# Kernel optimization log

Measured on AMD Instinct MI355X. Metric: run time of the kernel, lower is better.

## Reference

```python
import jax, jax.numpy as jnp
import numpy as np

LAN_DIM = 2048
FEA_DIM = 128
N = 65536
SHRINK_THRES = 0.0025
R = 1.0
EPS = 1e-12


def setup_inputs() -> dict:
    key = jax.random.key(0)
    k1, k2 = jax.random.split(key)
    x = jax.random.normal(k1, (N, FEA_DIM), dtype=jnp.float32)
    # reset_parameters: uniform(-stdv, stdv), stdv = 1/sqrt(fea_dim)
    stdv = 1.0 / np.sqrt(FEA_DIM)
    weight = jax.random.uniform(k2, (LAN_DIM, FEA_DIM), dtype=jnp.float32,
                                minval=-stdv, maxval=stdv)
    return {"input": x, "weight": weight}


def reference(input, weight):
    x = input                                    # [N, D]
    logits = jnp.einsum('nd,ld->nl', x, weight)  # [N, L]
    att = jax.nn.softmax(logits, axis=1)
    # hard_shrink_relu
    shifted = att - SHRINK_THRES
    att = jax.nn.relu(shifted) * att / (jnp.abs(shifted) + EPS)
    # F.normalize(p=1, dim=1): x / max(||x||_1, eps); att is nonneg
    att = att / jnp.maximum(jnp.sum(att, axis=1, keepdims=True), EPS)
    output = jnp.einsum('nl,ld->nd', att, weight)  # [N, D]

    # nearest landmark: argmax over att per sample
    ind = jnp.argmax(att, axis=1)                # [N]
    nl = weight[ind]                             # [N, D]
    # second-nearest: overwrite each row's argmax entry with the row min, re-argmax
    row_min = jnp.min(att, axis=1)               # [N]
    att2 = att.at[jnp.arange(N), ind].set(row_min)
    ind2 = jnp.argmax(att2, axis=1)
    nl2 = weight[ind2]                           # [N, D]

    # center of codebook, samples within radius R (boolean mask instead of
    # data-dependent-length index list, for jit compatibility)
    cen = jnp.mean(weight, axis=0)               # [D]
    dist = jnp.sqrt(jnp.sum((x - cen[None, :]) ** 2, axis=1))
    col = dist < R                               # [N] bool

    return output, att, nl, nl2, col
```

## Files before the change

kernel.cpp:

```cpp
#include <hip/hip_runtime.h>
#include <math.h>

#define NS 65536
#define LAN 2048
#define FEA 128

constexpr float THRES = 0.0025f;
constexpr float FEPS  = 1e-12f;
constexpr int BM   = 32;
constexpr int MAXS = 63;

typedef _Float16 half8 __attribute__((ext_vector_type(8)));
typedef float    f32x4 __attribute__((ext_vector_type(4)));

__global__ void k_prep(const float* __restrict__ W,
                       _Float16* __restrict__ Wh, _Float16* __restrict__ Wl,
                       float* __restrict__ cen) {
    if (blockIdx.x < 1024) {
        int i = blockIdx.x * 256 + threadIdx.x;
        float w = W[i];
        _Float16 h = (_Float16)w;
        Wh[i] = h;
        Wl[i] = (_Float16)(w - (float)h);
    } else {
        __shared__ float sb[4];
        int k = blockIdx.x - 1024;
        int tid = threadIdx.x;
        float s = 0.f;
        for (int c = tid; c < LAN; c += 256) s += W[(size_t)c * FEA + k];
        #pragma unroll
        for (int off = 32; off >= 1; off >>= 1) s += __shfl_xor(s, off);
        if ((tid & 63) == 0) sb[tid >> 6] = s;
        __syncthreads();
        if (tid == 0) cen[k] = (sb[0] + sb[1] + sb[2] + sb[3]) * (1.0f / (float)LAN);
    }
}

__device__ static inline void gload_lds16(const void* g, void* l) {
    __builtin_amdgcn_global_load_lds(
        (const __attribute__((address_space(1))) void*)g,
        (__attribute__((address_space(3))) void*)l, 16, 0, 0);
}

__global__ __launch_bounds__(512, 2) void k_main(
    const float* __restrict__ X,
    const _Float16* __restrict__ Wh, const _Float16* __restrict__ Wl,
    const float* __restrict__ cen,
    float* __restrict__ o_att, float* __restrict__ o_col)
{
    __shared__ __align__(16) char s_pool[147456];
    __shared__ float s_red[8][BM];
    __shared__ float s_rsinv[BM], s_Sinv[BM];
    __shared__ int   s_cnt[BM];

    const int tid  = threadIdx.x;
    const int wv   = tid >> 6;
    const int lane = tid & 63;
    const int g    = lane >> 4;
    const int m    = lane & 15;
    const int row0 = blockIdx.x * BM;
    constexpr int XOFF = 131072;

    #define ISSUE_B(t_, buf_)                                                        \
        {                                                                            \
            const char* gh_ = (const char*)(Wh + (size_t)(wv * 256 + (t_) * 16) * FEA); \
            const char* gl_ = (const char*)(Wl + (size_t)(wv * 256 + (t_) * 16) * FEA); \
            char* lb_ = s_pool + (buf_) * 65536 + wv * 8192;                         \
            _Pragma("unroll")                                                        \
            for (int i_ = 0; i_ < 4; ++i_) {                                         \
                int c_ = i_ * 64 + lane;                                             \
                int gc_ = c_ ^ ((c_ >> 4) & 7);                                      \
                gload_lds16(gh_ + gc_ * 16, lb_ + i_ * 1024);                        \
            }                                                                        \
            _Pragma("unroll")                                                        \
            for (int i_ = 0; i_ < 4; ++i_) {                                         \
                int c_ = i_ * 64 + lane;                                             \
                int gc_ = c_ ^ ((c_ >> 4) & 7);                                      \
                gload_lds16(gl_ + gc_ * 16, lb_ + 4096 + i_ * 1024);                 \
            }                                                                        \
        }

    {
        const char* xg = (const char*)(X + (size_t)row0 * FEA);
        gload_lds16(xg + (wv * 2 + 0) * 1024 + lane * 16, s_pool + XOFF + (wv * 2 + 0) * 1024);
        gload_lds16(xg + (wv * 2 + 1) * 1024 + lane * 16, s_pool + XOFF + (wv * 2 + 1) * 1024);
    }
    ISSUE_B(0, 0)
    ISSUE_B(1, 1)
    asm volatile("s_waitcnt vmcnt(16)" ::: "memory");
    __builtin_amdgcn_s_barrier();
    __builtin_amdgcn_sched_barrier(0);

    half8 afh[2][4], afl[2][4];
    #pragma unroll
    for (int rt = 0; rt < 2; ++rt)
        #pragma unroll
        for (int kb = 0; kb < 4; ++kb) {
            const char* base = s_pool + XOFF + (rt * 16 + m) * 512 + (kb * 8 + g * 2) * 16;
            f32x4 xa = *(const f32x4*)(base);
            f32x4 xb = *(const f32x4*)(base + 16);
            half8 h, l;
            #pragma unroll
            for (int e = 0; e < 4; ++e) {
                _Float16 hh = (_Float16)xa[e];
                h[e] = hh; l[e] = (_Float16)(xa[e] - (float)hh);
            }
            #pragma unroll
            for (int e = 0; e < 4; ++e) {
                _Float16 hh = (_Float16)xb[e];
                h[4 + e] = hh; l[4 + e] = (_Float16)(xb[e] - (float)hh);
            }
            afh[rt][kb] = h; afl[rt][kb] = l;
        }

    #pragma unroll
    for (int u = 0; u < 4; ++u) {
        const int lr = wv * 4 + u;
        float2 x2 = *(const float2*)(s_pool + XOFF + lr * 512 + lane * 8);
        float dx0 = x2.x - cen[lane * 2];
        float dx1 = x2.y - cen[lane * 2 + 1];
        float dd = dx0 * dx0 + dx1 * dx1;
        #pragma unroll
        for (int off = 32; off >= 1; off >>= 1) dd += __shfl_xor(dd, off);
        if (lane == 0) o_col[row0 + lr] = (sqrtf(dd) < 1.0f) ? 1.0f : 0.0f;
    }

    f32x4 acc[2][16];
    #pragma unroll
    for (int rt = 0; rt < 2; ++rt)
        #pragma unroll
        for (int t = 0; t < 16; ++t) acc[rt][t] = (f32x4){0.f, 0.f, 0.f, 0.f};
    float ssum[2][4];
    #pragma unroll
    for (int rt = 0; rt < 2; ++rt)
        #pragma unroll
        for (int r = 0; r < 4; ++r) ssum[rt][r] = 0.f;

    #pragma unroll 16
    for (int t = 0; t < 16; ++t) {
        const int buf = t & 1;
        const char* bb = s_pool + buf * 65536 + wv * 8192;
        if (t < 15) { asm volatile("s_waitcnt vmcnt(12)" ::: "memory"); }
        else        { asm volatile("s_waitcnt vmcnt(4)"  ::: "memory"); }
        __builtin_amdgcn_sched_barrier(0);
        half8 bh[4];
        #pragma unroll
        for (int kb = 0; kb < 4; ++kb) {
            int off = (m * 256 + kb * 64 + g * 16) ^ ((m & 7) << 4);
            bh[kb] = *(const half8*)(bb + off);
        }
        asm volatile("s_waitcnt lgkmcnt(0)" ::: "memory");
        __builtin_amdgcn_sched_barrier(0);
        __builtin_amdgcn_s_setprio(1);
        #pragma unroll
        for (int kb = 0; kb < 4; ++kb)
            #pragma unroll
            for (int rt = 0; rt < 2; ++rt) {
                acc[rt][t] = __builtin_amdgcn_mfma_f32_16x16x32_f16(afh[rt][kb], bh[kb], acc[rt][t], 0, 0, 0);
                acc[rt][t] = __builtin_amdgcn_mfma_f32_16x16x32_f16(afl[rt][kb], bh[kb], acc[rt][t], 0, 0, 0);
            }
        __builtin_amdgcn_s_setprio(0);
        if (t < 15) { asm volatile("s_waitcnt vmcnt(8)" ::: "memory"); }
        else        { asm volatile("s_waitcnt vmcnt(0)" ::: "memory"); }
        __builtin_amdgcn_sched_barrier(0);
        half8 bl[4];
        #pragma unroll
        for (int kb = 0; kb < 4; ++kb) {
            int off = (m * 256 + kb * 64 + g * 16) ^ ((m & 7) << 4);
            bl[kb] = *(const half8*)(bb + 4096 + off);
        }
        asm volatile("s_waitcnt lgkmcnt(0)" ::: "memory");
        __builtin_amdgcn_sched_barrier(0);
        if (t < 14) ISSUE_B(t + 2, buf)
        __builtin_amdgcn_s_setprio(1);
        #pragma unroll
        for (int kb = 0; kb < 4; ++kb)
            #pragma unroll
            for (int rt = 0; rt < 2; ++rt)
                acc[rt][t] = __builtin_amdgcn_mfma_f32_16x16x32_f16(afh[rt][kb], bl[kb], acc[rt][t], 0, 0, 0);
        __builtin_amdgcn_s_setprio(0);
        #pragma unroll
        for (int rt = 0; rt < 2; ++rt)
            #pragma unroll
            for (int r = 0; r < 4; ++r) {
                float e = __expf(acc[rt][t][r]);
                acc[rt][t][r] = e;
                ssum[rt][r] += e;
            }
    }
    #undef ISSUE_B


    #pragma unroll
    for (int rt = 0; rt < 2; ++rt)
        #pragma unroll
        for (int r = 0; r < 4; ++r) {
            float s = ssum[rt][r];
            #pragma unroll
            for (int off = 8; off >= 1; off >>= 1) s += __shfl_xor(s, off);
            if (m == 0) s_red[wv][rt*16 + g*4 + r] = s;
        }
    __syncthreads();
    if (tid < BM) {
        float s = s_red[0][tid];
        #pragma unroll
        for (int w = 1; w < 8; ++w) s += s_red[w][tid];
        s_rsinv[tid] = 1.0f / s;
        s_cnt[tid] = 0;
    }
    __syncthreads();

    int*   s_scol = (int*)s_pool;
    float* s_sval = (float*)(s_pool + 16384);
    #pragma unroll
    for (int rt = 0; rt < 2; ++rt)
        #pragma unroll
        for (int r = 0; r < 4; ++r) {
            const int lr = rt*16 + g*4 + r;
            const float ri = s_rsinv[lr];
            float S = 0.f;
            #pragma unroll
            for (int t = 0; t < 16; ++t) {
                float soft = acc[rt][t][r] * ri;
                float sh = soft - THRES;
                if (sh > 0.f) {
                    float v = sh * soft / (sh + FEPS);
                    S += v;
                    int p = atomicAdd(&s_cnt[lr], 1);
                    if (p < MAXS) { s_scol[lr*64 + p] = wv*256 + t*16 + m; s_sval[lr*64 + p] = v; }
                }
            }
            #pragma unroll
            for (int off = 8; off >= 1; off >>= 1) S += __shfl_xor(S, off);
            if (m == 0) s_red[wv][lr] = S;
        }
    __syncthreads();
    if (tid < BM) {
        float S = s_red[0][tid];
        #pragma unroll
        for (int w = 1; w < 8; ++w) S += s_red[w][tid];
        s_Sinv[tid] = 1.0f / fmaxf(S, FEPS);
    }
    __syncthreads();

    {
        const int lrp = tid >> 4, j = tid & 15;
        const int cn = min(s_cnt[lrp], MAXS);
        const float si = s_Sinv[lrp];
        f32x4 vq, cq;
        #pragma unroll
        for (int e = 0; e < 4; ++e) {
            int p = j * 4 + e;
            if (p == 63) {
                vq[e] = 0.f;
                cq[e] = __int_as_float(cn);
            } else {
                bool live = p < cn;
                vq[e] = live ? s_sval[lrp*64 + p] * si : 0.f;
                cq[e] = __int_as_float(live ? s_scol[lrp*64 + p] : 0);
            }
        }
        float* base = o_att + (size_t)(row0 + lrp) * LAN;
        *(f32x4*)(base + j * 4)      = vq;
        *(f32x4*)(base + 64 + j * 4) = cq;
    }
}

__global__ __launch_bounds__(256) void k_att(
    const float* __restrict__ W,
    float* __restrict__ o_att, float* __restrict__ o_out,
    float* __restrict__ o_nl, float* __restrict__ o_nl2)
{
    __shared__ float s_att[8 * 2048];
    __shared__ float s_pack[8][128];
    __shared__ int   s_i1[8], s_i2[8];

    const int tid = threadIdx.x;
    const size_t rows0 = (size_t)blockIdx.x * 8;
    const int row = tid >> 5, q = tid & 31;

    *(f32x4*)&s_pack[row][q * 4] = *(const f32x4*)(o_att + (rows0 + row) * LAN + q * 4);
    __syncthreads();

    if (tid < 8) {
        const float* pk = s_pack[tid];
        const int cnt = __float_as_int(pk[64 + 63]);
        float t1v = -1.f, t2v = -1.f; int t1c = 0x7fffffff, t2c = 0x7fffffff;
        for (int p = 0; p < cnt; ++p) {
            float v = pk[p]; int c = __float_as_int(pk[64 + p]);
            if (v > t1v || (v == t1v && c < t1c)) {
                t2v = t1v; t2c = t1c; t1v = v; t1c = c;
            } else if (v > t2v || (v == t2v && c < t2c)) {
                t2v = v; t2c = c;
            }
        }
        s_i1[tid] = (cnt >= 1) ? t1c : 0;
        s_i2[tid] = (cnt >= 2) ? t2c : 0;
    }
    f32x4* sa4 = (f32x4*)s_att;
    #pragma unroll
    for (int e = 0; e < 16; ++e) sa4[e * 256 + tid] = (f32x4){0.f, 0.f, 0.f, 0.f};
    __syncthreads();

    {
        const int cnt = __float_as_int(s_pack[row][64 + 63]);
        #pragma unroll
        for (int h = 0; h < 2; ++h) {
            int p = q + h * 32;
            if (p < cnt) {
                float v = s_pack[row][p];
                int c = __float_as_int(s_pack[row][64 + p]);
                s_att[row * 2048 + c] = v;
            }
        }
        f32x4 o = (f32x4){0.f, 0.f, 0.f, 0.f};
        for (int p = 0; p < cnt; ++p) {
            float v = s_pack[row][p];
            int c = __float_as_int(s_pack[row][64 + p]);
            const f32x4 w4 = *(const f32x4*)(W + (size_t)c * FEA + q * 4);
            o += v * w4;
        }
        *(f32x4*)(o_out + (rows0 + row) * FEA + q * 4) = o;
        const int i1 = s_i1[row], i2 = s_i2[row];
        *(f32x4*)(o_nl  + (rows0 + row) * FEA + q * 4) = *(const f32x4*)(W + (size_t)i1 * FEA + q * 4);
        *(f32x4*)(o_nl2 + (rows0 + row) * FEA + q * 4) = *(const f32x4*)(W + (size_t)i2 * FEA + q * 4);
    }
    __syncthreads();

    float* gdst = o_att + rows0 * LAN;
    #pragma unroll
    for (int e = 0; e < 16; ++e) {
        int fi = e * 256 + tid;
        *(f32x4*)(gdst + (size_t)fi * 4) = sa4[fi];
    }
}

extern "C" void kernel_launch(void* const* d_in, const int* in_sizes, int n_in,
                              void* d_out, int out_size, void* d_ws, size_t ws_size,
                              hipStream_t stream) {
    const float* X = (const float*)d_in[0];
    const float* W = (const float*)d_in[1];

    _Float16* Wh = (_Float16*)d_ws;
    _Float16* Wl = Wh + (size_t)LAN * FEA;
    float*    cen = (float*)(Wl + (size_t)LAN * FEA);

    float* out      = (float*)d_out;
    float* o_output = out;
    float* o_att    = o_output + (size_t)NS * FEA;
    float* o_nl     = o_att    + (size_t)NS * LAN;
    float* o_nl2    = o_nl     + (size_t)NS * FEA;
    float* o_col    = o_nl2    + (size_t)NS * FEA;

    k_prep<<<1152, 256, 0, stream>>>(W, Wh, Wl, cen);
    k_main<<<NS / BM, 512, 0, stream>>>(X, Wh, Wl, cen, o_att, o_col);
    k_att<<<NS / 8, 256, 0, stream>>>(W, o_att, o_output, o_nl, o_nl2);
}
```

Baseline: 311.4 us.

## Process two row tiles per block, shrink LDS, read Wl from global

Each k_main block now handles 64 rows in two passes of 32, so the grid is half as large. The low-half weight Wl is read straight from global memory into registers rather than staged in LDS. The input low parts are kept in LDS instead of registers, which cuts the shared-memory footprint from about 147KB to about 106KB and frees registers. The B-high prefetch for the second pass is issued early, and the final att store in k_att uses nontemporal stores. In exchange, the global Wl loads are uncached by LDS and repeated across waves, and the extra barriers per pass add synchronisation.

```diff
diff --git a/kernel.cpp b/kernel.cpp
--- a/kernel.cpp
+++ b/kernel.cpp
@@ -7,7 +7,6 @@
 
 constexpr float THRES = 0.0025f;
 constexpr float FEPS  = 1e-12f;
-constexpr int BM   = 32;
 constexpr int MAXS = 63;
 
 typedef _Float16 half8 __attribute__((ext_vector_type(8)));
@@ -42,228 +41,255 @@
         (__attribute__((address_space(3))) void*)l, 16, 0, 0);
 }
 
+#define RAWBAR() { asm volatile("s_waitcnt lgkmcnt(0)" ::: "memory"); \
+                   __builtin_amdgcn_s_barrier(); \
+                   __builtin_amdgcn_sched_barrier(0); }
+
 __global__ __launch_bounds__(512, 2) void k_main(
     const float* __restrict__ X,
     const _Float16* __restrict__ Wh, const _Float16* __restrict__ Wl,
     const float* __restrict__ cen,
     float* __restrict__ o_att, float* __restrict__ o_col)
 {
-    __shared__ __align__(16) char s_pool[147456];
-    __shared__ float s_red[8][BM];
-    __shared__ float s_rsinv[BM], s_Sinv[BM];
-    __shared__ int   s_cnt[BM];
+    __shared__ __align__(16) char s_pool[106496];
+    __shared__ float s_red[8][32];
+    __shared__ float s_rsinv[32], s_Sinv[32];
+    __shared__ int   s_cnt[32];
 
     const int tid  = threadIdx.x;
     const int wv   = tid >> 6;
     const int lane = tid & 63;
     const int g    = lane >> 4;
     const int m    = lane & 15;
-    const int row0 = blockIdx.x * BM;
-    constexpr int XOFF = 131072;
-
-    #define ISSUE_B(t_, buf_)                                                        \
-        {                                                                            \
+    constexpr int XR0 = 65536, XR1 = 81920, AFL = 98304;
+
+    #define ISSUE_BH(t_, buf_)                                                      \
+        {                                                                           \
             const char* gh_ = (const char*)(Wh + (size_t)(wv * 256 + (t_) * 16) * FEA); \
-            const char* gl_ = (const char*)(Wl + (size_t)(wv * 256 + (t_) * 16) * FEA); \
-            char* lb_ = s_pool + (buf_) * 65536 + wv * 8192;                         \
-            _Pragma("unroll")                                                        \
-            for (int i_ = 0; i_ < 4; ++i_) {                                         \
-                int c_ = i_ * 64 + lane;                                             \
-                int gc_ = c_ ^ ((c_ >> 4) & 7);                                      \
-                gload_lds16(gh_ + gc_ * 16, lb_ + i_ * 1024);                        \
-            }                                                                        \
-            _Pragma("unroll")                                                        \
-            for (int i_ = 0; i_ < 4; ++i_) {                                         \
-                int c_ = i_ * 64 + lane;                                             \
-                int gc_ = c_ ^ ((c_ >> 4) & 7);                                      \
-                gload_lds16(gl_ + gc_ * 16, lb_ + 4096 + i_ * 1024);                 \
-            }                                                                        \
+            char* lb_ = s_pool + (buf_) * 32768 + wv * 4096;                        \
+            _Pragma("unroll")                                                       \
+            for (int i_ = 0; i_ < 4; ++i_) {                                        \
+                int c_ = i_ * 64 + lane;                                            \
+                int gc_ = c_ ^ ((c_ >> 4) & 7);                                     \
+                gload_lds16(gh_ + gc_ * 16, lb_ + i_ * 1024);                       \
+            }                                                                       \
         }
 
     {
-        const char* xg = (const char*)(X + (size_t)row0 * FEA);
-        gload_lds16(xg + (wv * 2 + 0) * 1024 + lane * 16, s_pool + XOFF + (wv * 2 + 0) * 1024);
-        gload_lds16(xg + (wv * 2 + 1) * 1024 + lane * 16, s_pool + XOFF + (wv * 2 + 1) * 1024);
-    }
-    ISSUE_B(0, 0)
-    ISSUE_B(1, 1)
-    asm volatile("s_waitcnt vmcnt(16)" ::: "memory");
+        const char* xg = (const char*)(X + (size_t)blockIdx.x * 64 * FEA);
+        gload_lds16(xg + (wv * 2 + 0) * 1024 + lane * 16, s_pool + XR0 + (wv * 2 + 0) * 1024);
+        gload_lds16(xg + (wv * 2 + 1) * 1024 + lane * 16, s_pool + XR0 + (wv * 2 + 1) * 1024);
+        gload_lds16(xg + 16384 + (wv * 2 + 0) * 1024 + lane * 16, s_pool + XR1 + (wv * 2 + 0) * 1024);
+        gload_lds16(xg + 16384 + (wv * 2 + 1) * 1024 + lane * 16, s_pool + XR1 + (wv * 2 + 1) * 1024);
+    }
+    asm volatile("s_waitcnt vmcnt(2)" ::: "memory");
     __builtin_amdgcn_s_barrier();
     __builtin_amdgcn_sched_barrier(0);
 
-    half8 afh[2][4], afl[2][4];
-    #pragma unroll
-    for (int rt = 0; rt < 2; ++rt)
-        #pragma unroll
-        for (int kb = 0; kb < 4; ++kb) {
-            const char* base = s_pool + XOFF + (rt * 16 + m) * 512 + (kb * 8 + g * 2) * 16;
-            f32x4 xa = *(const f32x4*)(base);
-            f32x4 xb = *(const f32x4*)(base + 16);
-            half8 h, l;
+    for (int pass = 0; pass < 2; ++pass) {
+        const int row0 = blockIdx.x * 64 + pass * 32;
+        const int XR = pass ? XR1 : XR0;
+
+        half8 afh[2][4];
+        #pragma unroll
+        for (int rt = 0; rt < 2; ++rt)
+            #pragma unroll
+            for (int kb = 0; kb < 4; ++kb) {
+                const char* base = s_pool + XR + (rt * 16 + m) * 512 + (kb * 32 + g * 8) * 4;
+                f32x4 xa = *(const f32x4*)(base);
+                f32x4 xb = *(const f32x4*)(base + 16);
+                half8 h, l;
+                #pragma unroll
+                for (int e = 0; e < 4; ++e) {
+                    _Float16 hh = (_Float16)xa[e];
+                    h[e] = hh; l[e] = (_Float16)(xa[e] - (float)hh);
+                }
+                #pragma unroll
+                for (int e = 0; e < 4; ++e) {
+                    _Float16 hh = (_Float16)xb[e];
+                    h[4 + e] = hh; l[4 + e] = (_Float16)(xb[e] - (float)hh);
+                }
+                afh[rt][kb] = h;
+                int ab = (((rt * 16 + m) * 256 + kb * 64 + g * 16) ^ ((m & 7) << 4));
+                *(half8*)(s_pool + AFL + ab) = l;
+            }
+
+        #pragma unroll
+        for (int u = 0; u < 4; ++u) {
+            const int lr = wv * 4 + u;
+            float2 x2 = *(const float2*)(s_pool + XR + lr * 512 + lane * 8);
+            float dx0 = x2.x - cen[lane * 2];
+            float dx1 = x2.y - cen[lane * 2 + 1];
+            float dd = dx0 * dx0 + dx1 * dx1;
+            #pragma unroll
+            for (int off = 32; off >= 1; off >>= 1) dd += __shfl_xor(dd, off);
+            if (lane == 0) o_col[row0 + lr] = (sqrtf(dd) < 1.0f) ? 1.0f : 0.0f;
+        }
+
+        if (pass == 0) { ISSUE_BH(0, 0) ISSUE_BH(1, 1) }
+
+        f32x4 acc[2][16];
+        #pragma unroll
+        for (int rt = 0; rt < 2; ++rt)
+            #pragma unroll
+            for (int t = 0; t < 16; ++t) acc[rt][t] = (f32x4){0.f, 0.f, 0.f, 0.f};
+        float ssum[2][4];
+        #pragma unroll
+        for (int rt = 0; rt < 2; ++rt)
+            #pragma unroll
+            for (int r = 0; r < 4; ++r) ssum[rt][r] = 0.f;
+
+        #pragma unroll 16
+        for (int t = 0; t < 16; ++t) {
+            const int buf = t & 1;
+            __builtin_amdgcn_sched_barrier(0);
+            const _Float16* blp = Wl + (size_t)(wv * 256 + t * 16 + m) * FEA + g * 8;
+            half8 bl0v = *(const half8*)(blp);
+            half8 bl1v = *(const half8*)(blp + 32);
+            half8 bl2v = *(const half8*)(blp + 64);
+            half8 bl3v = *(const half8*)(blp + 96);
+            __builtin_amdgcn_sched_barrier(0);
+            if (t == 15) { asm volatile("s_waitcnt vmcnt(4)" ::: "memory"); }
+            else         { asm volatile("s_waitcnt vmcnt(8)" ::: "memory"); }
+            __builtin_amdgcn_sched_barrier(0);
+            const char* bb = s_pool + buf * 32768 + wv * 4096;
+            half8 bh0v, bh1v, bh2v, bh3v;
+            {
+                int o0 = (m * 256 + 0 * 64 + g * 16) ^ ((m & 7) << 4);
+                int o1 = (m * 256 + 1 * 64 + g * 16) ^ ((m & 7) << 4);
+                int o2 = (m * 256 + 2 * 64 + g * 16) ^ ((m & 7) << 4);
+                int o3 = (m * 256 + 3 * 64 + g * 16) ^ ((m & 7) << 4);
+                bh0v = *(const half8*)(bb + o0);
+                bh1v = *(const half8*)(bb + o1);
+                bh2v = *(const half8*)(bb + o2);
+                bh3v = *(const half8*)(bb + o3);
+            }
+            asm volatile("s_waitcnt lgkmcnt(0)" ::: "memory");
+            __builtin_amdgcn_sched_barrier(0);
+            if (t < 14) ISSUE_BH(t + 2, buf)
+            half8 l00 = *(const half8*)(s_pool + AFL + (((0 * 16 + m) * 256 + 0 * 64 + g * 16) ^ ((m & 7) << 4)));
+            half8 l01 = *(const half8*)(s_pool + AFL + (((0 * 16 + m) * 256 + 1 * 64 + g * 16) ^ ((m & 7) << 4)));
+            half8 l02 = *(const half8*)(s_pool + AFL + (((0 * 16 + m) * 256 + 2 * 64 + g * 16) ^ ((m & 7) << 4)));
+            half8 l03 = *(const half8*)(s_pool + AFL + (((0 * 16 + m) * 256 + 3 * 64 + g * 16) ^ ((m & 7) << 4)));
+            half8 l10 = *(const half8*)(s_pool + AFL + (((1 * 16 + m) * 256 + 0 * 64 + g * 16) ^ ((m & 7) << 4)));
+            half8 l11 = *(const half8*)(s_pool + AFL + (((1 * 16 + m) * 256 + 1 * 64 + g * 16) ^ ((m & 7) << 4)));
+            half8 l12 = *(const half8*)(s_pool + AFL + (((1 * 16 + m) * 256 + 2 * 64 + g * 16) ^ ((m & 7) << 4)));
+            half8 l13 = *(const half8*)(s_pool + AFL + (((1 * 16 + m) * 256 + 3 * 64 + g * 16) ^ ((m & 7) << 4)));
+            __builtin_amdgcn_s_setprio(1);
+            acc[0][t] = __builtin_amdgcn_mfma_f32_16x16x32_f16(afh[0][0], bh0v, acc[0][t], 0, 0, 0);
+            acc[1][t] = __builtin_amdgcn_mfma_f32_16x16x32_f16(afh[1][0], bh0v, acc[1][t], 0, 0, 0);
+            acc[0][t] = __builtin_amdgcn_mfma_f32_16x16x32_f16(afh[0][1], bh1v, acc[0][t], 0, 0, 0);
+            acc[1][t] = __builtin_amdgcn_mfma_f32_16x16x32_f16(afh[1][1], bh1v, acc[1][t], 0, 0, 0);
+            acc[0][t] = __builtin_amdgcn_mfma_f32_16x16x32_f16(afh[0][2], bh2v, acc[0][t], 0, 0, 0);
+            acc[1][t] = __builtin_amdgcn_mfma_f32_16x16x32_f16(afh[1][2], bh2v, acc[1][t], 0, 0, 0);
+            acc[0][t] = __builtin_amdgcn_mfma_f32_16x16x32_f16(afh[0][3], bh3v, acc[0][t], 0, 0, 0);
+            acc[1][t] = __builtin_amdgcn_mfma_f32_16x16x32_f16(afh[1][3], bh3v, acc[1][t], 0, 0, 0);
+            acc[0][t] = __builtin_amdgcn_mfma_f32_16x16x32_f16(l00, bh0v, acc[0][t], 0, 0, 0);
+            acc[1][t] = __builtin_amdgcn_mfma_f32_16x16x32_f16(l10, bh0v, acc[1][t], 0, 0, 0);
+            acc[0][t] = __builtin_amdgcn_mfma_f32_16x16x32_f16(l01, bh1v, acc[0][t], 0, 0, 0);
+            acc[1][t] = __builtin_amdgcn_mfma_f32_16x16x32_f16(l11, bh1v, acc[1][t], 0, 0, 0);
+            acc[0][t] = __builtin_amdgcn_mfma_f32_16x16x32_f16(l02, bh2v, acc[0][t], 0, 0, 0);
+            acc[1][t] = __builtin_amdgcn_mfma_f32_16x16x32_f16(l12, bh2v, acc[1][t], 0, 0, 0);
+            acc[0][t] = __builtin_amdgcn_mfma_f32_16x16x32_f16(l03, bh3v, acc[0][t], 0, 0, 0);
+            acc[1][t] = __builtin_amdgcn_mfma_f32_16x16x32_f16(l13, bh3v, acc[1][t], 0, 0, 0);
+            acc[0][t] = __builtin_amdgcn_mfma_f32_16x16x32_f16(afh[0][0], bl0v, acc[0][t], 0, 0, 0);
+            acc[1][t] = __builtin_amdgcn_mfma_f32_16x16x32_f16(afh[1][0], bl0v, acc[1][t], 0, 0, 0);
+            acc[0][t] = __builtin_amdgcn_mfma_f32_16x16x32_f16(afh[0][1], bl1v, acc[0][t], 0, 0, 0);
+            acc[1][t] = __builtin_amdgcn_mfma_f32_16x16x32_f16(afh[1][1], bl1v, acc[1][t], 0, 0, 0);
+            acc[0][t] = __builtin_amdgcn_mfma_f32_16x16x32_f16(afh[0][2], bl2v, acc[0][t], 0, 0, 0);
+            acc[1][t] = __builtin_amdgcn_mfma_f32_16x16x32_f16(afh[1][2], bl2v, acc[1][t], 0, 0, 0);
+            acc[0][t] = __builtin_amdgcn_mfma_f32_16x16x32_f16(afh[0][3], bl3v, acc[0][t], 0, 0, 0);
+            acc[1][t] = __builtin_amdgcn_mfma_f32_16x16x32_f16(afh[1][3], bl3v, acc[1][t], 0, 0, 0);
+            __builtin_amdgcn_s_setprio(0);
+            #pragma unroll
+            for (int rt = 0; rt < 2; ++rt)
+                #pragma unroll
+                for (int r = 0; r < 4; ++r) {
+                    float e = __expf(acc[rt][t][r]);
+                    acc[rt][t][r] = e;
+                    ssum[rt][r] += e;
+                }
+        }
+
+        if (pass == 0) { ISSUE_BH(0, 0) ISSUE_BH(1, 1) }
+
+
+        #pragma unroll
+        for (int rt = 0; rt < 2; ++rt)
+            #pragma unroll
+            for (int r = 0; r < 4; ++r) {
+                float s = ssum[rt][r];
+                #pragma unroll
+                for (int off = 8; off >= 1; off >>= 1) s += __shfl_xor(s, off);
+                if (m == 0) s_red[wv][rt * 16 + g * 4 + r] = s;
+            }
+        RAWBAR();
+        if (tid < 32) {
+            float s = s_red[0][tid];
+            #pragma unroll
+            for (int w = 1; w < 8; ++w) s += s_red[w][tid];
+            s_rsinv[tid] = 1.0f / s;
+            s_cnt[tid] = 0;
+        }
+        RAWBAR();
+
+        int*   s_scol = (int*)(s_pool + XR0);
+        float* s_sval = (float*)(s_pool + XR0 + 8192);
+        #pragma unroll
+        for (int rt = 0; rt < 2; ++rt)
+            #pragma unroll
+            for (int r = 0; r < 4; ++r) {
+                const int lr = rt * 16 + g * 4 + r;
+                const float ri = s_rsinv[lr];
+                float S = 0.f;
+                #pragma unroll
+                for (int t = 0; t < 16; ++t) {
+                    float soft = acc[rt][t][r] * ri;
+                    float sh = soft - THRES;
+                    if (sh > 0.f) {
+                        float v = sh * soft / (sh + FEPS);
+                        S += v;
+                        int p = atomicAdd(&s_cnt[lr], 1);
+                        if (p < MAXS) { s_scol[lr * 64 + p] = wv * 256 + t * 16 + m; s_sval[lr * 64 + p] = v; }
+                    }
+                }
+                #pragma unroll
+                for (int off = 8; off >= 1; off >>= 1) S += __shfl_xor(S, off);
+                if (m == 0) s_red[wv][lr] = S;
+            }
+        RAWBAR();
+        if (tid < 32) {
+            float S = s_red[0][tid];
+            #pragma unroll
+            for (int w = 1; w < 8; ++w) S += s_red[w][tid];
+            s_Sinv[tid] = 1.0f / fmaxf(S, FEPS);
+        }
+        RAWBAR();
+
+        {
+            const int lrp = tid >> 4, j = tid & 15;
+            const int cn = min(s_cnt[lrp], MAXS);
+            const float si = s_Sinv[lrp];
+            f32x4 vq, cq;
             #pragma unroll
             for (int e = 0; e < 4; ++e) {
-                _Float16 hh = (_Float16)xa[e];
-                h[e] = hh; l[e] = (_Float16)(xa[e] - (float)hh);
-            }
-            #pragma unroll
-            for (int e = 0; e < 4; ++e) {
-                _Float16 hh = (_Float16)xb[e];
-                h[4 + e] = hh; l[4 + e] = (_Float16)(xb[e] - (float)hh);
-            }
-            afh[rt][kb] = h; afl[rt][kb] = l;
-        }
-
-    #pragma unroll
-    for (int u = 0; u < 4; ++u) {
-        const int lr = wv * 4 + u;
-        float2 x2 = *(const float2*)(s_pool + XOFF + lr * 512 + lane * 8);
-        float dx0 = x2.x - cen[lane * 2];
-        float dx1 = x2.y - cen[lane * 2 + 1];
-        float dd = dx0 * dx0 + dx1 * dx1;
-        #pragma unroll
-        for (int off = 32; off >= 1; off >>= 1) dd += __shfl_xor(dd, off);
-        if (lane == 0) o_col[row0 + lr] = (sqrtf(dd) < 1.0f) ? 1.0f : 0.0f;
-    }
-
-    f32x4 acc[2][16];
-    #pragma unroll
-    for (int rt = 0; rt < 2; ++rt)
-        #pragma unroll
-        for (int t = 0; t < 16; ++t) acc[rt][t] = (f32x4){0.f, 0.f, 0.f, 0.f};
-    float ssum[2][4];
-    #pragma unroll
-    for (int rt = 0; rt < 2; ++rt)
-        #pragma unroll
-        for (int r = 0; r < 4; ++r) ssum[rt][r] = 0.f;
-
-    #pragma unroll 16
-    for (int t = 0; t < 16; ++t) {
-        const int buf = t & 1;
-        const char* bb = s_pool + buf * 65536 + wv * 8192;
-        if (t < 15) { asm volatile("s_waitcnt vmcnt(12)" ::: "memory"); }
-        else        { asm volatile("s_waitcnt vmcnt(4)"  ::: "memory"); }
-        __builtin_amdgcn_sched_barrier(0);
-        half8 bh[4];
-        #pragma unroll
-        for (int kb = 0; kb < 4; ++kb) {
-            int off = (m * 256 + kb * 64 + g * 16) ^ ((m & 7) << 4);
-            bh[kb] = *(const half8*)(bb + off);
-        }
-        asm volatile("s_waitcnt lgkmcnt(0)" ::: "memory");
-        __builtin_amdgcn_sched_barrier(0);
-        __builtin_amdgcn_s_setprio(1);
-        #pragma unroll
-        for (int kb = 0; kb < 4; ++kb)
-            #pragma unroll
-            for (int rt = 0; rt < 2; ++rt) {
-                acc[rt][t] = __builtin_amdgcn_mfma_f32_16x16x32_f16(afh[rt][kb], bh[kb], acc[rt][t], 0, 0, 0);
-                acc[rt][t] = __builtin_amdgcn_mfma_f32_16x16x32_f16(afl[rt][kb], bh[kb], acc[rt][t], 0, 0, 0);
-            }
-        __builtin_amdgcn_s_setprio(0);
-        if (t < 15) { asm volatile("s_waitcnt vmcnt(8)" ::: "memory"); }
-        else        { asm volatile("s_waitcnt vmcnt(0)" ::: "memory"); }
-        __builtin_amdgcn_sched_barrier(0);
-        half8 bl[4];
-        #pragma unroll
-        for (int kb = 0; kb < 4; ++kb) {
-            int off = (m * 256 + kb * 64 + g * 16) ^ ((m & 7) << 4);
-            bl[kb] = *(const half8*)(bb + 4096 + off);
-        }
-        asm volatile("s_waitcnt lgkmcnt(0)" ::: "memory");
-        __builtin_amdgcn_sched_barrier(0);
-        if (t < 14) ISSUE_B(t + 2, buf)
-        __builtin_amdgcn_s_setprio(1);
-        #pragma unroll
-        for (int kb = 0; kb < 4; ++kb)
-            #pragma unroll
-            for (int rt = 0; rt < 2; ++rt)
-                acc[rt][t] = __builtin_amdgcn_mfma_f32_16x16x32_f16(afh[rt][kb], bl[kb], acc[rt][t], 0, 0, 0);
-        __builtin_amdgcn_s_setprio(0);
-        #pragma unroll
-        for (int rt = 0; rt < 2; ++rt)
-            #pragma unroll
-            for (int r = 0; r < 4; ++r) {
-                float e = __expf(acc[rt][t][r]);
-                acc[rt][t][r] = e;
-                ssum[rt][r] += e;
-            }
-    }
-    #undef ISSUE_B
-
-
-    #pragma unroll
-    for (int rt = 0; rt < 2; ++rt)
-        #pragma unroll
-        for (int r = 0; r < 4; ++r) {
-            float s = ssum[rt][r];
-            #pragma unroll
-            for (int off = 8; off >= 1; off >>= 1) s += __shfl_xor(s, off);
-            if (m == 0) s_red[wv][rt*16 + g*4 + r] = s;
-        }
-    __syncthreads();
-    if (tid < BM) {
-        float s = s_red[0][tid];
-        #pragma unroll
-        for (int w = 1; w < 8; ++w) s += s_red[w][tid];
-        s_rsinv[tid] = 1.0f / s;
-        s_cnt[tid] = 0;
-    }
-    __syncthreads();
-
-    int*   s_scol = (int*)s_pool;
-    float* s_sval = (float*)(s_pool + 16384);
-    #pragma unroll
-    for (int rt = 0; rt < 2; ++rt)
-        #pragma unroll
-        for (int r = 0; r < 4; ++r) {
-            const int lr = rt*16 + g*4 + r;
-            const float ri = s_rsinv[lr];
-            float S = 0.f;
-            #pragma unroll
-            for (int t = 0; t < 16; ++t) {
-                float soft = acc[rt][t][r] * ri;
-                float sh = soft - THRES;
-                if (sh > 0.f) {
-                    float v = sh * soft / (sh + FEPS);
-                    S += v;
-                    int p = atomicAdd(&s_cnt[lr], 1);
-                    if (p < MAXS) { s_scol[lr*64 + p] = wv*256 + t*16 + m; s_sval[lr*64 + p] = v; }
-                }
-            }
-            #pragma unroll
-            for (int off = 8; off >= 1; off >>= 1) S += __shfl_xor(S, off);
-            if (m == 0) s_red[wv][lr] = S;
-        }
-    __syncthreads();
-    if (tid < BM) {
-        float S = s_red[0][tid];
-        #pragma unroll
-        for (int w = 1; w < 8; ++w) S += s_red[w][tid];
-        s_Sinv[tid] = 1.0f / fmaxf(S, FEPS);
-    }
-    __syncthreads();
-
-    {
-        const int lrp = tid >> 4, j = tid & 15;
-        const int cn = min(s_cnt[lrp], MAXS);
-        const float si = s_Sinv[lrp];
-        f32x4 vq, cq;
-        #pragma unroll
-        for (int e = 0; e < 4; ++e) {
-            int p = j * 4 + e;
-            if (p == 63) {
-                vq[e] = 0.f;
-                cq[e] = __int_as_float(cn);
-            } else {
-                bool live = p < cn;
-                vq[e] = live ? s_sval[lrp*64 + p] * si : 0.f;
-                cq[e] = __int_as_float(live ? s_scol[lrp*64 + p] : 0);
-            }
-        }
-        float* base = o_att + (size_t)(row0 + lrp) * LAN;
-        *(f32x4*)(base + j * 4)      = vq;
-        *(f32x4*)(base + 64 + j * 4) = cq;
-    }
+                int p = j * 4 + e;
+                if (p == 63) {
+                    vq[e] = 0.f;
+                    cq[e] = __int_as_float(cn);
+                } else {
+                    bool live = p < cn;
+                    vq[e] = live ? s_sval[lrp * 64 + p] * si : 0.f;
+                    cq[e] = __int_as_float(live ? s_scol[lrp * 64 + p] : 0);
+                }
+            }
+            float* base = o_att + (size_t)(row0 + lrp) * LAN;
+            *(f32x4*)(base + j * 4)      = vq;
+            *(f32x4*)(base + 64 + j * 4) = cq;
+        }
+        RAWBAR();
+    }
+    #undef ISSUE_BH
 }
 
 __global__ __launch_bounds__(256) void k_att(
@@ -331,7 +357,7 @@
     #pragma unroll
     for (int e = 0; e < 16; ++e) {
         int fi = e * 256 + tid;
-        *(f32x4*)(gdst + (size_t)fi * 4) = sa4[fi];
+        __builtin_nontemporal_store(sa4[fi], (f32x4*)(gdst + (size_t)fi * 4));
     }
 }
 
@@ -353,6 +379,6 @@
     float* o_col    = o_nl2    + (size_t)NS * FEA;
 
     k_prep<<<1152, 256, 0, stream>>>(W, Wh, Wl, cen);
-    k_main<<<NS / BM, 512, 0, stream>>>(X, Wh, Wl, cen, o_att, o_col);
+    k_main<<<NS / 64, 512, 0, stream>>>(X, Wh, Wl, cen, o_att, o_col);
     k_att<<<NS / 8, 256, 0, stream>>>(W, o_att, o_output, o_nl, o_nl2);
 }
```

New measurement: 801.2 us. +157.3%, slower.
